# Optimization experiments

Measured on AMD Instinct MI355X. Metric: run time of the kernel, lower is better.

The kernel has to match this reference:

```python
import jax, jax.numpy as jnp
import numpy as np

TIME_BIN = 8.0            # ms, pr_params['timeBin']
DT = 0.001 * TIME_BIN     # TimeStep in seconds


def _rieke(x, sigma, phi, eta, cgmp2cur, cgmphill, cdark, beta, betaSlow,
           hillcoef, hillaffinity, gamma, gdark):
    # x: (B, T, P); params: (1, 1) broadcast over (B, P)
    darkCurrent = gdark ** cgmphill * cgmp2cur / 2
    gdark_ = (2 * darkCurrent / cgmp2cur) ** (1.0 / cgmphill)
    cur2ca = beta * cdark / darkCurrent
    smax = eta / phi * gdark_ * (1 + (cdark / hillaffinity) ** hillcoef)

    B, T, P = x.shape
    ones = jnp.ones((B, P), x.dtype)
    g0 = gdark_ * ones
    s0 = gdark_ * eta / phi * ones
    c0 = cdark * ones
    cs0 = cdark * ones
    r0 = x[:, 0, :] * gamma / sigma
    p0 = (eta + r0) / phi * ones

    def step(carry, x_t):
        g, s, c, cs, r, p = carry
        r1 = r + DT * (-sigma * r) + gamma * x_t
        p1 = p + DT * (r + eta - phi * p)
        c1 = c + DT * (cur2ca * cgmp2cur * g ** cgmphill / (1 + cs / cdark) - beta * c)
        cs1 = cs - DT * (betaSlow * (cs - c))
        s1 = smax / (1 + (c1 / hillaffinity) ** hillcoef)
        g1 = g + DT * (s - p * g)
        return (g1, s1, c1, cs1, r1, p1), g1

    xs = jnp.moveaxis(x[:, :-1, :], 1, 0)  # (T-1, B, P): step pnt uses x[:, pnt-1]
    _, gs = jax.lax.scan(step, (g0, s0, c0, cs0, r0, p0), xs)
    g_all = jnp.concatenate([jnp.zeros((1, B, P), x.dtype), gs], axis=0)  # g[0] = 0
    g_all = jnp.moveaxis(g_all, 0, 1)  # (B, T, P)
    return -(cgmp2cur * g_all ** cgmphill) / 2


def setup_inputs() -> dict:
    key = jax.random.key(0)
    B, T, P = 16, 1000, 2500
    x = jax.random.uniform(key, (B, T, P), dtype=jnp.float32)
    p11 = lambda v: jnp.full((1, 1), v, dtype=jnp.float32)
    return {
        'x': x,
        'sigma': p11(22.0), 'phi': p11(22.0), 'eta': p11(2000.0),
        'cgmp2cur': p11(0.01), 'cgmphill': p11(3.0), 'cdark': p11(1.0),
        'beta': p11(9.0), 'betaSlow': p11(0.4), 'hillcoef': p11(4.0),
        'hillaffinity': p11(0.5), 'gamma': p11(10.0), 'gdark': p11(20.0),
    }


def reference(x, sigma, phi, eta, cgmp2cur, cgmphill, cdark, beta, betaSlow,
              hillcoef, hillaffinity, gamma, gdark):
    # call() scales gamma by 1/timeBin (all scaleFacs are 1.0)
    gamma_eff = gamma / TIME_BIN
    return _rieke(x, sigma, phi, eta, cgmp2cur, cgmphill, cdark, beta,
                  betaSlow, hillcoef, hillaffinity, gamma_eff, gdark)
```

## Files before the change

### kernel.cpp

```cpp
#include <hip/hip_runtime.h>

#define B_ 16
#define T_ 1000
#define P_ 2500
#define NCH (B_ * P_)

#define AS1 __attribute__((address_space(1)))
#define AS3 __attribute__((address_space(3)))

__device__ __forceinline__ float rcp_fast(float v) {
    return __builtin_amdgcn_rcpf(v);
}

extern "C" __global__ void __launch_bounds__(64, 1)
prk_kernel(const float* __restrict__ x,
           const float* __restrict__ sigma_p,  const float* __restrict__ phi_p,
           const float* __restrict__ eta_p,    const float* __restrict__ c2c_p,
           const float* __restrict__ hill_p,   const float* __restrict__ cdark_p,
           const float* __restrict__ beta_p,   const float* __restrict__ bslow_p,
           const float* __restrict__ hcoef_p,  const float* __restrict__ haff_p,
           const float* __restrict__ gamma_p,  const float* __restrict__ gdark_p,
           float* __restrict__ out)
{
    const int lane = threadIdx.x;
    const int cid  = blockIdx.x * 64 + lane;
    const int b    = cid / P_;
    const int p    = cid - b * P_;

    const float sigma        = sigma_p[0];
    const float phi          = phi_p[0];
    const float eta          = eta_p[0];
    const float cgmp2cur     = c2c_p[0];
    const float cgmphill     = hill_p[0];
    const float cdark        = cdark_p[0];
    const float beta         = beta_p[0];
    const float betaSlow     = bslow_p[0];
    const float hillcoef     = hcoef_p[0];
    const float hillaffinity = haff_p[0];
    const float gamma        = gamma_p[0] * 0.125f;
    const float gdark        = gdark_p[0];
    const float DT = 0.008f;

    const float darkCurrent = powf(gdark, cgmphill) * cgmp2cur * 0.5f;
    const float gdark_ = powf(2.0f * darkCurrent / cgmp2cur, 1.0f / cgmphill);
    const float cur2ca = beta * cdark / darkCurrent;
    const float smax   = eta / phi * gdark_ *
                         (1.0f + powf(cdark / hillaffinity, hillcoef));

    const float Ar  = 1.0f - DT * sigma;
    const float Ap  = 1.0f - DT * phi;
    const float Pe  = DT * eta;
    const float Ac  = 1.0f - DT * beta;
    const float Kc  = DT * cur2ca * cgmp2cur;
    const float Acs = 1.0f - DT * betaSlow;
    const float Bcs = DT * betaSlow;
    const float inv_cd = 1.0f / cdark;
    const float inv_ha = 1.0f / hillaffinity;
    const float outk   = -0.5f * cgmp2cur;

    const float* __restrict__ xrow = x   + (size_t)b * T_ * P_ + p;
    float*       __restrict__ op   = out + (size_t)b * T_ * P_ + p;

    float r  = xrow[0] * gamma / sigma;
    float pv = (eta + r) / phi;
    float g  = gdark_;
    float g3 = gdark_ * gdark_ * gdark_;
    float s  = gdark_ * eta / phi;
    float c  = cdark;
    float cs = cdark;
    op[0] = 0.0f;

    if (cgmphill == 3.0f && hillcoef == 4.0f) {
        __shared__ float xlds[3][16][64];

#define WAITV(n) do {                                                    \
            asm volatile("s_waitcnt vmcnt(" #n ")" ::: "memory");        \
            __builtin_amdgcn_sched_barrier(0);                           \
        } while (0)
#define STAGE(ck) do {                                                   \
            const int _bi = (ck) % 3;                                    \
            _Pragma("unroll")                                            \
            for (int _u = 0; _u < 16; ++_u) {                            \
                int _tt = 16 * (ck) + _u;                                \
                _tt = _tt > 998 ? 998 : _tt;                             \
                __builtin_amdgcn_global_load_lds(                        \
                    (const AS1 void*)(const void*)(xrow + (size_t)_tt * P_), \
                    (AS3 void*)(void*)&xlds[_bi][_u][0], 4, 0, 0);       \
            }                                                            \
        } while (0)
#define COMP(ck, nst) do {                                               \
            const int _bi = (ck) % 3;                                    \
            _Pragma("unroll")                                            \
            for (int _u = 0; _u < (nst); ++_u) {                         \
                float xt  = xlds[_bi][_u][lane];                         \
                float r1  = fmaf(Ar, r, gamma * xt);                     \
                float p1  = fmaf(Ap, pv, fmaf(DT, r, Pe));               \
                float den = fmaf(cs, inv_cd, 1.0f);                      \
                float c1  = fmaf(Ac, c, Kc * g3 * rcp_fast(den));        \
                float cs1 = fmaf(Acs, cs, Bcs * c);                      \
                float yy  = c1 * inv_ha;                                 \
                float y2  = yy * yy;                                     \
                float s1  = smax * rcp_fast(fmaf(y2, y2, 1.0f));         \
                float g1  = fmaf(DT, fmaf(-pv, g, s), g);                \
                float g1c = (g1 * g1) * g1;                              \
                __builtin_nontemporal_store(outk * g1c,                  \
                    op + (size_t)(16 * (ck) + _u + 1) * P_);             \
                r = r1; pv = p1; c = c1; cs = cs1; s = s1;               \
                g = g1; g3 = g1c;                                        \
            }                                                            \
        } while (0)

        STAGE(0); STAGE(1);
        WAITV(16); COMP(0, 16); STAGE(2);
        #pragma unroll 1
        for (int kk = 1; kk <= 58; kk += 3) {
            WAITV(32); COMP(kk,     16); STAGE(kk + 2);
            WAITV(32); COMP(kk + 1, 16); STAGE(kk + 3);
            WAITV(32); COMP(kk + 2, 16); STAGE(kk + 4);
        }
        WAITV(32); COMP(61, 16);
        WAITV(16); COMP(62, 7);

#undef WAITV
#undef STAGE
#undef COMP
    } else {
        for (int t = 0; t < T_ - 1; ++t) {
            float xt  = xrow[(size_t)t * P_];
            float r1  = r + DT * (-sigma * r) + gamma * xt;
            float p1  = pv + DT * (r + eta - phi * pv);
            float c1  = c + DT * (cur2ca * cgmp2cur * powf(g, cgmphill) /
                                  (1.0f + cs / cdark) - beta * c);
            float cs1 = cs - DT * (betaSlow * (cs - c));
            float s1  = smax / (1.0f + powf(c1 / hillaffinity, hillcoef));
            float g1  = g + DT * (s - pv * g);
            op[(size_t)(t + 1) * P_] = -(cgmp2cur * powf(g1, cgmphill)) * 0.5f;
            r = r1; pv = p1; c = c1; cs = cs1; s = s1; g = g1;
        }
    }
}

extern "C" void kernel_launch(void* const* d_in, const int* in_sizes, int n_in,
                              void* d_out, int out_size, void* d_ws, size_t ws_size,
                              hipStream_t stream) {
    const float* x = (const float*)d_in[0];
    prk_kernel<<<dim3(NCH / 64), dim3(64), 0, stream>>>(
        x,
        (const float*)d_in[1],  (const float*)d_in[2],  (const float*)d_in[3],
        (const float*)d_in[4],  (const float*)d_in[5],  (const float*)d_in[6],
        (const float*)d_in[7],  (const float*)d_in[8],  (const float*)d_in[9],
        (const float*)d_in[10], (const float*)d_in[11], (const float*)d_in[12],
        (float*)d_out);
}
```

Baseline: 73.02 us.

## Split compute and output-store into producer/consumer waves via LDS double buffer

Each block now runs two waves: wave 0 runs the sequential recurrence and writes its results into a double-buffered LDS output tile, while wave 1 flushes those tiles to global memory as 16-byte vectorized nontemporal stores. The aim is to take the scattered scalar per-step global stores off the serial dependency chain and widen the writes. It adds a block barrier per 16-step chunk and extra LDS traffic, and the compute wave now has to read its inputs from LDS into registers before each chunk.

```diff
diff --git a/kernel.cpp b/kernel.cpp
--- a/kernel.cpp
+++ b/kernel.cpp
@@ -7,12 +7,13 @@
 
 #define AS1 __attribute__((address_space(1)))
 #define AS3 __attribute__((address_space(3)))
+typedef float f4 __attribute__((ext_vector_type(4)));
 
 __device__ __forceinline__ float rcp_fast(float v) {
     return __builtin_amdgcn_rcpf(v);
 }
 
-extern "C" __global__ void __launch_bounds__(64, 1)
+extern "C" __global__ void __launch_bounds__(128, 1)
 prk_kernel(const float* __restrict__ x,
            const float* __restrict__ sigma_p,  const float* __restrict__ phi_p,
            const float* __restrict__ eta_p,    const float* __restrict__ c2c_p,
@@ -22,10 +23,8 @@
            const float* __restrict__ gamma_p,  const float* __restrict__ gdark_p,
            float* __restrict__ out)
 {
-    const int lane = threadIdx.x;
-    const int cid  = blockIdx.x * 64 + lane;
-    const int b    = cid / P_;
-    const int p    = cid - b * P_;
+    const int lane = threadIdx.x & 63;
+    const int wv   = threadIdx.x >> 6;
 
     const float sigma        = sigma_p[0];
     const float phi          = phi_p[0];
@@ -58,41 +57,67 @@
     const float inv_ha = 1.0f / hillaffinity;
     const float outk   = -0.5f * cgmp2cur;
 
+    const int cid = blockIdx.x * 64 + lane;
+    const int b   = cid / P_;
+    const int p   = cid - b * P_;
     const float* __restrict__ xrow = x   + (size_t)b * T_ * P_ + p;
-    float*       __restrict__ op   = out + (size_t)b * T_ * P_ + p;
-
-    float r  = xrow[0] * gamma / sigma;
-    float pv = (eta + r) / phi;
-    float g  = gdark_;
-    float g3 = gdark_ * gdark_ * gdark_;
-    float s  = gdark_ * eta / phi;
-    float c  = cdark;
-    float cs = cdark;
-    op[0] = 0.0f;
+    float*       __restrict__ oprt = out + (size_t)b * T_ * P_ + p;
+
+    const int colg = (lane & 15) * 4;
+    const int rowl = lane >> 4;
+    const int cidL = blockIdx.x * 64 + colg;
+    const int b_l  = cidL / P_;
+    const int p_l  = cidL - b_l * P_;
+    float* __restrict__ old_ = out + (size_t)b_l * T_ * P_ + p_l;
+
+    __shared__ float xlds[3][16][64];
+    __shared__ float obuf[2][16][64];
 
     if (cgmphill == 3.0f && hillcoef == 4.0f) {
-        __shared__ float xlds[3][16][64];
+
+#define SYNC() do {                                                      \
+            asm volatile("s_waitcnt lgkmcnt(0)" ::: "memory");           \
+            __builtin_amdgcn_sched_barrier(0);                           \
+            __builtin_amdgcn_s_barrier();                                \
+            __builtin_amdgcn_sched_barrier(0);                           \
+        } while (0)
+
+        if (wv == 0) {
+            float r  = xrow[0] * gamma / sigma;
+            float pv = (eta + r) / phi;
+            float g  = gdark_;
+            float g3 = gdark_ * gdark_ * gdark_;
+            float s  = gdark_ * eta / phi;
+            float c  = cdark;
+            float cs = cdark;
+            float vx[16];
 
 #define WAITV(n) do {                                                    \
             asm volatile("s_waitcnt vmcnt(" #n ")" ::: "memory");        \
             __builtin_amdgcn_sched_barrier(0);                           \
         } while (0)
 #define STAGE(ck) do {                                                   \
-            const int _bi = (ck) % 3;                                    \
+            float* _dst = &xlds[(ck) % 3][0][0];                         \
             _Pragma("unroll")                                            \
             for (int _u = 0; _u < 16; ++_u) {                            \
                 int _tt = 16 * (ck) + _u;                                \
                 _tt = _tt > 998 ? 998 : _tt;                             \
                 __builtin_amdgcn_global_load_lds(                        \
                     (const AS1 void*)(const void*)(xrow + (size_t)_tt * P_), \
-                    (AS3 void*)(void*)&xlds[_bi][_u][0], 4, 0, 0);       \
+                    (AS3 void*)(void*)(_dst + _u * 64), 4, 0, 0);        \
             }                                                            \
         } while (0)
-#define COMP(ck, nst) do {                                               \
-            const int _bi = (ck) % 3;                                    \
+#define READC(bi) do {                                                   \
+            _Pragma("unroll")                                            \
+            for (int _u = 0; _u < 16; ++_u)                              \
+                vx[_u] = xlds[bi][_u][lane];                             \
+            asm volatile("s_waitcnt lgkmcnt(0)" ::: "memory");           \
+            __builtin_amdgcn_sched_barrier(0);                           \
+        } while (0)
+#define COMP(ob, nst) do {                                               \
             _Pragma("unroll")                                            \
             for (int _u = 0; _u < (nst); ++_u) {                         \
-                float xt  = xlds[_bi][_u][lane];                         \
+                float xt  = vx[_u];                                      \
                 float r1  = fmaf(Ar, r, gamma * xt);                     \
                 float p1  = fmaf(Ap, pv, fmaf(DT, r, Pe));               \
                 float den = fmaf(cs, inv_cd, 1.0f);                      \
@@ -103,28 +128,68 @@
                 float s1  = smax * rcp_fast(fmaf(y2, y2, 1.0f));         \
                 float g1  = fmaf(DT, fmaf(-pv, g, s), g);                \
                 float g1c = (g1 * g1) * g1;                              \
-                __builtin_nontemporal_store(outk * g1c,                  \
-                    op + (size_t)(16 * (ck) + _u + 1) * P_);             \
+                obuf[ob][_u][lane] = outk * g1c;                         \
                 r = r1; pv = p1; c = c1; cs = cs1; s = s1;               \
                 g = g1; g3 = g1c;                                        \
             }                                                            \
         } while (0)
 
-        STAGE(0); STAGE(1);
-        WAITV(16); COMP(0, 16); STAGE(2);
-        #pragma unroll 1
-        for (int kk = 1; kk <= 58; kk += 3) {
-            WAITV(32); COMP(kk,     16); STAGE(kk + 2);
-            WAITV(32); COMP(kk + 1, 16); STAGE(kk + 3);
-            WAITV(32); COMP(kk + 2, 16); STAGE(kk + 4);
-        }
-        WAITV(32); COMP(61, 16);
-        WAITV(16); COMP(62, 7);
-
+            STAGE(0); STAGE(1);
+            int bi = 0, ob = 0;
+            #pragma unroll 1
+            for (int k = 0; k <= 60; ++k) {
+                WAITV(16);
+                READC(bi);
+                COMP(ob, 16);
+                STAGE(k + 2);
+                SYNC();
+                bi = (bi == 2) ? 0 : bi + 1;
+                ob ^= 1;
+            }
+            WAITV(16); READC(bi); COMP(ob, 16); SYNC();
+            bi = (bi == 2) ? 0 : bi + 1;  ob ^= 1;
+            WAITV(0);  READC(bi); COMP(ob, 7);  SYNC();
 #undef WAITV
 #undef STAGE
+#undef READC
 #undef COMP
+        } else {
+#define FLUSH(ck, ob, nrow) do {                                         \
+            _Pragma("unroll")                                            \
+            for (int _i = 0; _i < 4; ++_i) {                             \
+                const int _rr = rowl + 4 * _i;                           \
+                if (_rr < (nrow)) {                                      \
+                    f4 _v = *(const f4*)&obuf[ob][_rr][colg];            \
+                    __builtin_nontemporal_store(_v,                      \
+                        (f4*)(old_ + (size_t)(16 * (ck) + 1 + _rr) * P_)); \
+                }                                                        \
+            }                                                            \
+        } while (0)
+            if (lane < 16) {
+                f4 z = {0.0f, 0.0f, 0.0f, 0.0f};
+                __builtin_nontemporal_store(z, (f4*)old_);
+            }
+            SYNC();
+            int ob = 0;
+            #pragma unroll 1
+            for (int k = 1; k <= 62; ++k) {
+                FLUSH(k - 1, ob, 16);
+                SYNC();
+                ob ^= 1;
+            }
+            FLUSH(62, ob, 7);
+#undef FLUSH
+        }
+#undef SYNC
     } else {
+        if (wv != 0) return;
+        float r  = xrow[0] * gamma / sigma;
+        float pv = (eta + r) / phi;
+        float g  = gdark_;
+        float s  = gdark_ * eta / phi;
+        float c  = cdark;
+        float cs = cdark;
+        oprt[0] = 0.0f;
         for (int t = 0; t < T_ - 1; ++t) {
             float xt  = xrow[(size_t)t * P_];
             float r1  = r + DT * (-sigma * r) + gamma * xt;
@@ -134,7 +199,7 @@
             float cs1 = cs - DT * (betaSlow * (cs - c));
             float s1  = smax / (1.0f + powf(c1 / hillaffinity, hillcoef));
             float g1  = g + DT * (s - pv * g);
-            op[(size_t)(t + 1) * P_] = -(cgmp2cur * powf(g1, cgmphill)) * 0.5f;
+            oprt[(size_t)(t + 1) * P_] = -(cgmp2cur * powf(g1, cgmphill)) * 0.5f;
             r = r1; pv = p1; c = c1; cs = cs1; s = s1; g = g1;
         }
     }
@@ -144,7 +209,7 @@
                               void* d_out, int out_size, void* d_ws, size_t ws_size,
                               hipStream_t stream) {
     const float* x = (const float*)d_in[0];
-    prk_kernel<<<dim3(NCH / 64), dim3(64), 0, stream>>>(
+    prk_kernel<<<dim3(NCH / 64), dim3(128), 0, stream>>>(
         x,
         (const float*)d_in[1],  (const float*)d_in[2],  (const float*)d_in[3],
         (const float*)d_in[4],  (const float*)d_in[5],  (const float*)d_in[6],
```

After: 81.29 us. 11.3% more time.
